# Optimization experiments

Measured on AMD Instinct MI355X. Metric: run time of the kernel, lower is better.

The kernel has to match this reference:

```python
import jax, jax.numpy as jnp
import numpy as np

N_NODES = 50000
N_EDGES = 600000
VOCAB = 50000
D_IN = 256   # embed.output_size
D = 128      # size


def gcn_conv(x, w, b, src, dst, num_nodes):
    # PyG GCNConv: x' = D^{-1/2} (A + I) D^{-1/2} (x @ W^T) + b
    loop = jnp.arange(num_nodes)
    s = jnp.concatenate([src, loop])
    d = jnp.concatenate([dst, loop])
    x = x @ w.T                                           # [N, D]
    deg = jax.ops.segment_sum(jnp.ones_like(s, x.dtype), d, num_segments=num_nodes)
    dinv = jnp.where(deg > 0, jax.lax.rsqrt(deg), 0.0)
    norm = dinv[s] * dinv[d]                              # [E+N]
    msgs = x[s] * norm[:, None]                           # gather + scale
    out = jax.ops.segment_sum(msgs, d, num_segments=num_nodes)  # scatter-add
    return out + b


def setup_inputs() -> dict:
    key = jax.random.key(0)
    ks = jax.random.split(key, 7)
    node_tokens = jax.random.randint(ks[0], (N_NODES,), 0, VOCAB)
    edge_index = jax.random.randint(ks[1], (2, N_EDGES), 0, N_NODES)
    embed_table = jax.random.normal(ks[2], (VOCAB, D_IN), dtype=jnp.float32) * 0.02
    W_node_w = jax.random.normal(ks[3], (D, D_IN), dtype=jnp.float32) * 0.02
    W_node_b = jnp.zeros((D,), dtype=jnp.float32)
    w1 = jax.random.normal(ks[4], (D, D), dtype=jnp.float32) * 0.02
    b1 = jnp.zeros((D,), dtype=jnp.float32)
    w2 = jax.random.normal(ks[5], (D, D), dtype=jnp.float32) * 0.02
    b2 = jnp.zeros((D,), dtype=jnp.float32)
    return {"node_tokens": node_tokens, "edge_index": edge_index,
            "embed_table": embed_table, "W_node_w": W_node_w, "W_node_b": W_node_b,
            "w1": w1, "b1": b1, "w2": w2, "b2": b2}


def reference(node_tokens, edge_index, embed_table, W_node_w, W_node_b, w1, b1, w2, b2):
    src, dst = edge_index[0], edge_index[1]
    e = embed_table[node_tokens]                 # [N, D_IN] embedding lookup
    x = e @ W_node_w.T + W_node_b                # [N, D]
    x = gcn_conv(x, w1, b1, src, dst, N_NODES)
    x = jax.nn.relu(x)
    x = gcn_conv(x, w2, b2, src, dst, N_NODES)
    return x
```

## Files before the change

kernel.cpp:

```cpp
#include <hip/hip_runtime.h>
#include <hip/hip_bf16.h>

#define N_NODES 50000
#define N_EDGES 600000
#define D_IN 256
#define D 128

#define SCAN_CHUNK 1024
#define N_CHUNKS ((N_NODES + SCAN_CHUNK - 1) / SCAN_CHUNK)
#define GEMM_BLOCKS ((N_NODES + 31) / 32)
#define EDGE_BLOCKS ((N_EDGES + 255) / 256)

typedef unsigned short ushort_t;
typedef __attribute__((ext_vector_type(8))) short bf16x8;
typedef __attribute__((ext_vector_type(16))) float f32x16;

__device__ __forceinline__ float bf2f(ushort_t u) {
  union { unsigned int i; float f; } v;
  v.i = ((unsigned int)u) << 16;
  return v.f;
}
__device__ __forceinline__ ushort_t f2bf(float f) {
  union { float f; unsigned int i; } v;
  v.f = f;
  unsigned int x = v.i;
  unsigned int r = (x + 0x7FFFu + ((x >> 16) & 1u)) >> 16;
  return (ushort_t)r;
}


__global__ __launch_bounds__(256) void k_prep_deg(
    const float* __restrict__ wn, const float* __restrict__ w1,
    const float* __restrict__ bn, const float* __restrict__ w2,
    const float* __restrict__ b1, const float* __restrict__ b2,
    const int* __restrict__ dst,
    ushort_t* __restrict__ WcSw, float* __restrict__ bc,
    ushort_t* __restrict__ W2Sw, float* __restrict__ b1f,
    float* __restrict__ b2f, int* __restrict__ deg,
    int* __restrict__ epos) {
  int bid = blockIdx.x;
  if (bid < 128) {
    int j = bid;
    int k = threadIdx.x;
    float acc = 0.f;
    for (int m = 0; m < 128; m++)
      acc += w1[j * 128 + m] * wn[m * 256 + k];
    ushort_t h = f2bf(acc);
    ushort_t l = f2bf(acc - bf2f(h));
    int wv = j >> 5, fm = j & 31;
    int kh = k >> 7, t = (k >> 4) & 7, fq = (k >> 3) & 1, c = k & 7;
    int lane = fq * 32 + fm;
    int base = ((wv * 2 + kh) * 8 + t) * 2 * 512 + lane * 8 + c;
    WcSw[base] = h;
    WcSw[base + 512] = l;
    if (k == 0) {
      float s = 0.f;
      for (int m = 0; m < 128; m++) s += w1[j * 128 + m] * bn[m];
      bc[j] = s;
    }
  } else if (bid < 193) {
    int i = (bid - 128) * 256 + threadIdx.x;
    if (i >= 16640) return;
    if (i < 16384) {
      float v = w2[i];
      ushort_t h = f2bf(v);
      ushort_t l = f2bf(v - bf2f(h));
      int j = i >> 7, k = i & 127;
      int wv = j >> 5, fm = j & 31;
      int t = (k >> 4) & 7, fq = (k >> 3) & 1, c = k & 7;
      int lane = fq * 32 + fm;
      int base = (wv * 8 + t) * 2 * 512 + lane * 8 + c;
      W2Sw[base] = h;
      W2Sw[base + 512] = l;
    } else if (i < 16512) {
      b1f[i - 16384] = b1[i - 16384];
    } else {
      b2f[i - 16512] = b2[i - 16512];
    }
  } else {
    int e = (bid - 193) * 256 + threadIdx.x;
    if (e < N_EDGES) epos[e] = atomicAdd(&deg[dst[e]], 1);
  }
}


__global__ void k_partial(const int* __restrict__ deg, int* __restrict__ partial) {
  __shared__ int lds[256];
  int b = blockIdx.x, t = threadIdx.x;
  int base = b * SCAN_CHUNK + t * 4;
  int s = 0;
#pragma unroll
  for (int i = 0; i < 4; i++) {
    int idx = base + i;
    if (idx < N_NODES) s += deg[idx];
  }
  lds[t] = s;
  __syncthreads();
  for (int off = 128; off > 0; off >>= 1) {
    if (t < off) lds[t] += lds[t + off];
    __syncthreads();
  }
  if (t == 0) partial[b] = lds[0];
}

__global__ void k_scan_final(const int* __restrict__ deg, const int* __restrict__ partial,
                             int* __restrict__ row_start, float* __restrict__ dinv) {
  __shared__ int lds[256];
  __shared__ int plds[64];
  int b = blockIdx.x, t = threadIdx.x;
  if (t < N_CHUNKS) plds[t] = partial[t];
  __syncthreads();
  if (t == 0) {
    int s = 0;
    for (int i = 0; i < b; i++) s += plds[i];
    plds[63] = s;
  }
  int base = b * SCAN_CHUNK + t * 4;
  int v[4];
  int s = 0;
#pragma unroll
  for (int i = 0; i < 4; i++) {
    int idx = base + i;
    v[i] = (idx < N_NODES) ? deg[idx] : 0;
    s += v[i];
  }
  lds[t] = s;
  __syncthreads();
  for (int off = 1; off < 256; off <<= 1) {
    int add = (t >= off) ? lds[t - off] : 0;
    __syncthreads();
    lds[t] += add;
    __syncthreads();
  }
  int excl = lds[t] - s + plds[63];
#pragma unroll
  for (int i = 0; i < 4; i++) {
    int idx = base + i;
    if (idx < N_NODES) {
      row_start[idx] = excl;
      dinv[idx] = rsqrtf((float)(v[i] + 1));
      excl += v[i];
    }
  }
  if (b == 0 && t == 0) row_start[N_NODES] = N_EDGES;
}

__global__ __launch_bounds__(256) void k_gemm_fill(
    const float* __restrict__ Xv, const int* __restrict__ tokens,
    const ushort_t* __restrict__ Wsw,
    const float* __restrict__ bias, const float* __restrict__ dinvp,
    ushort_t* __restrict__ OutT,
    const int* __restrict__ src, const int* __restrict__ dst,
    const int* __restrict__ row_start, const int* __restrict__ epos,
    int* __restrict__ csr) {
  constexpr int KDIM = D_IN;
  constexpr int KH = KDIM / 128;
  constexpr int XS = KDIM + 8;
  __shared__ __align__(16) ushort_t xh_lds[32 * XS];
  __shared__ __align__(16) ushort_t xl_lds[32 * XS];

  int bid = blockIdx.x;
  if (bid >= GEMM_BLOCKS) {
    int e = (bid - GEMM_BLOCKS) * 256 + threadIdx.x;
    if (e < N_EDGES) {
      int d = dst[e];
      csr[row_start[d] + epos[e]] = src[e];
    }
    return;
  }

  int tid = threadIdx.x;
  int lane = tid & 63;
  int wv = tid >> 6;
  int node0 = bid * 32;
  int fm = lane & 31;
  int fq = lane >> 5;

  {
    constexpr int NT = (32 * KDIM / 4) / 256;
    float4 v[NT];
    int rows[NT], cs[NT];
#pragma unroll
    for (int i = 0; i < NT; i++) {
      int seg = tid + 256 * i;
      rows[i] = seg / (KDIM / 4);
      cs[i] = seg % (KDIM / 4);
      int tk = tokens[min(node0 + rows[i], N_NODES - 1)];
      v[i] = *(const float4*)&Xv[(size_t)tk * KDIM + 4 * cs[i]];
    }
#pragma unroll
    for (int i = 0; i < NT; i++) {
      ushort4 h, l;
      h.x = f2bf(v[i].x); l.x = f2bf(v[i].x - bf2f(h.x));
      h.y = f2bf(v[i].y); l.y = f2bf(v[i].y - bf2f(h.y));
      h.z = f2bf(v[i].z); l.z = f2bf(v[i].z - bf2f(h.z));
      h.w = f2bf(v[i].w); l.w = f2bf(v[i].w - bf2f(h.w));
      *(ushort4*)&xh_lds[rows[i] * XS + 4 * cs[i]] = h;
      *(ushort4*)&xl_lds[rows[i] * XS + 4 * cs[i]] = l;
    }
  }
  __syncthreads();

  f32x16 acc;
#pragma unroll
  for (int r = 0; r < 16; r++) acc[r] = 0.f;

#pragma unroll
  for (int kh = 0; kh < KH; kh++) {
    const ushort_t* wb = Wsw + ((size_t)(wv * KH + kh) * 8) * 2 * 512 + lane * 8;
    bf16x8 wbh[8], wbl[8];
#pragma unroll
    for (int t = 0; t < 8; t++) {
      wbh[t] = *(const bf16x8*)(wb + (size_t)t * 1024);
      wbl[t] = *(const bf16x8*)(wb + (size_t)t * 1024 + 512);
    }
#pragma unroll
    for (int t = 0; t < 8; t++) {
      int ko = kh * 128 + t * 16 + fq * 8;
      bf16x8 ah = *(const bf16x8*)&xh_lds[fm * XS + ko];
      bf16x8 al = *(const bf16x8*)&xl_lds[fm * XS + ko];
      acc = __builtin_amdgcn_mfma_f32_32x32x16_bf16(ah, wbh[t], acc, 0, 0, 0);
      acc = __builtin_amdgcn_mfma_f32_32x32x16_bf16(ah, wbl[t], acc, 0, 0, 0);
      acc = __builtin_amdgcn_mfma_f32_32x32x16_bf16(al, wbh[t], acc, 0, 0, 0);
    }
  }
  int j = wv * 32 + fm;
  float bv = bias[j];
#pragma unroll
  for (int r = 0; r < 16; r++) {
    int row = (r & 3) + 8 * (r >> 2) + 4 * fq;
    int node = node0 + row;
    if (node < N_NODES)
      OutT[(size_t)node * D + j] = f2bf((acc[r] + bv) * dinvp[node]);
  }
}

__device__ __forceinline__ void addu4(float acc[8], uint4 u) {
  acc[0] += bf2f((ushort_t)(u.x & 0xFFFFu));
  acc[1] += bf2f((ushort_t)(u.x >> 16));
  acc[2] += bf2f((ushort_t)(u.y & 0xFFFFu));
  acc[3] += bf2f((ushort_t)(u.y >> 16));
  acc[4] += bf2f((ushort_t)(u.z & 0xFFFFu));
  acc[5] += bf2f((ushort_t)(u.z >> 16));
  acc[6] += bf2f((ushort_t)(u.w & 0xFFFFu));
  acc[7] += bf2f((ushort_t)(u.w >> 16));
}

__device__ __forceinline__ void agg_group(
    const uint4* __restrict__ tu4, const int* __restrict__ csr,
    int e0, int e1, int lane, int h, float acc[8]) {
  int gbase = lane & 48;
  for (int base = e0; base < e1; base += 16) {
    int cnt = min(16, e1 - base);
    int sidx = (h < cnt) ? csr[base + h] : 0;
    int i = 0;
    for (; i + 8 <= cnt; i += 8) {
      uint4 u[8];
#pragma unroll
      for (int q = 0; q < 8; q++) {
        int s = __shfl(sidx, gbase + i + q);
        u[q] = tu4[(size_t)s * 16 + h];
      }
#pragma unroll
      for (int q = 0; q < 8; q++) addu4(acc, u[q]);
    }
    if (i + 4 <= cnt) {
      uint4 u[4];
#pragma unroll
      for (int q = 0; q < 4; q++) {
        int s = __shfl(sidx, gbase + i + q);
        u[q] = tu4[(size_t)s * 16 + h];
      }
#pragma unroll
      for (int q = 0; q < 4; q++) addu4(acc, u[q]);
      i += 4;
    }
    if (i + 2 <= cnt) {
      uint4 u[2];
#pragma unroll
      for (int q = 0; q < 2; q++) {
        int s = __shfl(sidx, gbase + i + q);
        u[q] = tu4[(size_t)s * 16 + h];
      }
      addu4(acc, u[0]);
      addu4(acc, u[1]);
      i += 2;
    }
    if (i < cnt) {
      int s = __shfl(sidx, gbase + i);
      uint4 u = tu4[(size_t)s * 16 + h];
      addu4(acc, u);
    }
  }
}

__global__ __launch_bounds__(256) void k_agg_gemm(
    const ushort_t* __restrict__ t1, const int* __restrict__ row_start,
    const int* __restrict__ csr, const float* __restrict__ dinv,
    const float* __restrict__ b1f,
    const ushort_t* __restrict__ Wsw, ushort_t* __restrict__ OutT2) {
  constexpr int XS = 136;
  __shared__ __align__(16) ushort_t xh_lds[32 * XS];
  __shared__ __align__(16) ushort_t xl_lds[32 * XS];

  int tid = threadIdx.x;
  int lane = tid & 63;
  int wv = tid >> 6;
  int node0 = blockIdx.x * 32;
  int fm = lane & 31;
  int fq = lane >> 5;
  int g = lane >> 4;
  int h = lane & 15;

  const uint4* tu4 = (const uint4*)t1;
  float4 bA = *(const float4*)&b1f[h * 8];
  float4 bB = *(const float4*)&b1f[h * 8 + 4];

  int node0w = node0 + wv * 8;
  int rsv = row_start[min(node0w + min(lane, 8), N_NODES)];

#pragma unroll
  for (int p = 0; p < 2; p++) {
    int r = p * 4 + g;
    int row = wv * 8 + r;
    int node = node0 + row;
    int e0 = __shfl(rsv, r);
    int e1 = __shfl(rsv, r + 1);
    float acc[8];
#pragma unroll
    for (int q = 0; q < 8; q++) acc[q] = 0.f;
    if (node < N_NODES) {
      agg_group(tu4, csr, e0, e1, lane, h, acc);
      addu4(acc, tu4[(size_t)node * 16 + h]);
    }
    bf16x8 ph, pl;
    if (node < N_NODES) {
      float di = dinv[node];
      float v[8];
      v[0] = fmaxf(di * acc[0] + bA.x, 0.f);
      v[1] = fmaxf(di * acc[1] + bA.y, 0.f);
      v[2] = fmaxf(di * acc[2] + bA.z, 0.f);
      v[3] = fmaxf(di * acc[3] + bA.w, 0.f);
      v[4] = fmaxf(di * acc[4] + bB.x, 0.f);
      v[5] = fmaxf(di * acc[5] + bB.y, 0.f);
      v[6] = fmaxf(di * acc[6] + bB.z, 0.f);
      v[7] = fmaxf(di * acc[7] + bB.w, 0.f);
#pragma unroll
      for (int q = 0; q < 8; q++) {
        ushort_t hq = f2bf(v[q]);
        ph[q] = (short)hq;
        pl[q] = (short)f2bf(v[q] - bf2f(hq));
      }
    } else {
#pragma unroll
      for (int q = 0; q < 8; q++) { ph[q] = 0; pl[q] = 0; }
    }
    *(bf16x8*)&xh_lds[row * XS + h * 8] = ph;
    *(bf16x8*)&xl_lds[row * XS + h * 8] = pl;
  }
  __syncthreads();

  f32x16 acc;
#pragma unroll
  for (int r = 0; r < 16; r++) acc[r] = 0.f;
  {
    const ushort_t* wb = Wsw + ((size_t)wv * 8) * 2 * 512 + lane * 8;
    bf16x8 wbh[8], wbl[8];
#pragma unroll
    for (int t = 0; t < 8; t++) {
      wbh[t] = *(const bf16x8*)(wb + (size_t)t * 1024);
      wbl[t] = *(const bf16x8*)(wb + (size_t)t * 1024 + 512);
    }
#pragma unroll
    for (int t = 0; t < 8; t++) {
      int ko = t * 16 + fq * 8;
      bf16x8 ah = *(const bf16x8*)&xh_lds[fm * XS + ko];
      bf16x8 al = *(const bf16x8*)&xl_lds[fm * XS + ko];
      acc = __builtin_amdgcn_mfma_f32_32x32x16_bf16(ah, wbh[t], acc, 0, 0, 0);
      acc = __builtin_amdgcn_mfma_f32_32x32x16_bf16(ah, wbl[t], acc, 0, 0, 0);
      acc = __builtin_amdgcn_mfma_f32_32x32x16_bf16(al, wbh[t], acc, 0, 0, 0);
    }
  }
  int j = wv * 32 + fm;
#pragma unroll
  for (int r = 0; r < 16; r++) {
    int row = (r & 3) + 8 * (r >> 2) + 4 * fq;
    int node = node0 + row;
    if (node < N_NODES)
      OutT2[(size_t)node * D + j] = f2bf(acc[r] * dinv[node]);
  }
}

__global__ __launch_bounds__(256) void k_aggregate_out(
    const ushort_t* __restrict__ t, const int* __restrict__ row_start,
    const int* __restrict__ csr, const float* __restrict__ dinv,
    const float* __restrict__ bias, float* __restrict__ out_f) {
  int wv = threadIdx.x >> 6;
  int lane = threadIdx.x & 63;
  int g = lane >> 4;
  int h = lane & 15;
  int nodew = blockIdx.x * 16 + wv * 4;
  int rsv = row_start[min(nodew + min(lane, 4), N_NODES)];
  int node = nodew + g;
  int e0 = __shfl(rsv, g);
  int e1 = __shfl(rsv, g + 1);
  if (node >= N_NODES) return;

  const uint4* tu4 = (const uint4*)t;
  float acc[8];
#pragma unroll
  for (int q = 0; q < 8; q++) acc[q] = 0.f;
  agg_group(tu4, csr, e0, e1, lane, h, acc);
  addu4(acc, tu4[(size_t)node * 16 + h]);
  float di = dinv[node];
  float4 bA = *(const float4*)&bias[h * 8];
  float4 bB = *(const float4*)&bias[h * 8 + 4];
  float4 o0, o1;
  o0.x = di * acc[0] + bA.x;
  o0.y = di * acc[1] + bA.y;
  o0.z = di * acc[2] + bA.z;
  o0.w = di * acc[3] + bA.w;
  o1.x = di * acc[4] + bB.x;
  o1.y = di * acc[5] + bB.y;
  o1.z = di * acc[6] + bB.z;
  o1.w = di * acc[7] + bB.w;
  *(float4*)&out_f[(size_t)node * D + h * 8] = o0;
  *(float4*)&out_f[(size_t)node * D + h * 8 + 4] = o1;
}

extern "C" void kernel_launch(void* const* d_in, const int* in_sizes, int n_in,
                              void* d_out, int out_size, void* d_ws, size_t ws_size,
                              hipStream_t stream) {
  const int* tokens = (const int*)d_in[0];
  const int* edge = (const int*)d_in[1];
  const float* embed = (const float*)d_in[2];
  const float* Wn = (const float*)d_in[3];
  const float* bn = (const float*)d_in[4];
  const float* w1 = (const float*)d_in[5];
  const float* b1 = (const float*)d_in[6];
  const float* w2 = (const float*)d_in[7];
  const float* b2 = (const float*)d_in[8];
  float* out = (float*)d_out;

  const int* src = edge;
  const int* dst = edge + N_EDGES;

  char* ws = (char*)d_ws;
  ushort_t* T1 = (ushort_t*)ws;
  ushort_t* T2 = (ushort_t*)(ws + 12800000);
  int* epos = (int*)(ws + 25600000);
  float* dinv = (float*)(ws + 38400000);
  int* row_start = (int*)(ws + 38600064);
  int* deg = (int*)(ws + 38800128);
  int* csr = (int*)(ws + 39200128);
  int* partial = (int*)(ws + 41600192);
  ushort_t* WcSw = (ushort_t*)(ws + 41600512);
  ushort_t* W2Sw = (ushort_t*)(ws + 41731584);
  float* bias_ws = (float*)(ws + 41797120);
  float* bcf = bias_ws;
  float* b1f = bias_ws + 128;
  float* b2f = bias_ws + 256;

  hipMemsetAsync(deg, 0, N_NODES * sizeof(int), stream);
  k_prep_deg<<<193 + EDGE_BLOCKS, 256, 0, stream>>>(
      Wn, w1, bn, w2, b1, b2, dst, WcSw, bcf, W2Sw, b1f, b2f, deg, epos);

  k_partial<<<N_CHUNKS, 256, 0, stream>>>(deg, partial);
  k_scan_final<<<N_CHUNKS, 256, 0, stream>>>(deg, partial, row_start, dinv);

  k_gemm_fill<<<GEMM_BLOCKS + EDGE_BLOCKS, 256, 0, stream>>>(
      embed, tokens, WcSw, bcf, dinv, T1, src, dst, row_start, epos, csr);

  k_agg_gemm<<<GEMM_BLOCKS, 256, 0, stream>>>(
      T1, row_start, csr, dinv, b1f, W2Sw, T2);

  k_aggregate_out<<<(N_NODES + 15) / 16, 256, 0, stream>>>(
      T2, row_start, csr, dinv, b2f, out);
}
```

Measured before the change: 232.3 us.

## Add zero sentinel rows and unconditional 16-wide gather bursts in aggregation

Adds a zero padding row at index N_NODES in T1 and T2, written by the scan kernel, so aggregation can always issue a full 16-edge burst of gathers and pad missing edges with the sentinel index. The variable-length 8/4/2/1 gather tail is removed. Self-loop rows, dinv and CSR indices are prefetched up front, and the two nodes per group in k_agg_gemm are processed with independent accumulators. The embedding GEMM now splits its K dimension into two 128-wide LDS halves, which halves LDS use at the cost of an extra barrier. Bf16 unpacking uses cheaper mask/shift helpers. The risk is wasted bandwidth on padded loads for low-degree nodes and higher register pressure.

```diff
diff --git a/kernel.cpp b/kernel.cpp
--- a/kernel.cpp
+++ b/kernel.cpp
@@ -26,6 +26,16 @@
   unsigned int x = v.i;
   unsigned int r = (x + 0x7FFFu + ((x >> 16) & 1u)) >> 16;
   return (ushort_t)r;
+}
+__device__ __forceinline__ float bflo(unsigned int u) {
+  union { unsigned int i; float f; } v;
+  v.i = u << 16;
+  return v.f;
+}
+__device__ __forceinline__ float bfhi(unsigned int u) {
+  union { unsigned int i; float f; } v;
+  v.i = u & 0xFFFF0000u;
+  return v.f;
 }
 
 
@@ -104,7 +114,8 @@
 }
 
 __global__ void k_scan_final(const int* __restrict__ deg, const int* __restrict__ partial,
-                             int* __restrict__ row_start, float* __restrict__ dinv) {
+                             int* __restrict__ row_start, float* __restrict__ dinv,
+                             ushort_t* __restrict__ T1z, ushort_t* __restrict__ T2z) {
   __shared__ int lds[256];
   __shared__ int plds[64];
   int b = blockIdx.x, t = threadIdx.x;
@@ -142,7 +153,13 @@
       excl += v[i];
     }
   }
-  if (b == 0 && t == 0) row_start[N_NODES] = N_EDGES;
+  if (b == 0) {
+    if (t == 0) row_start[N_NODES] = N_EDGES;
+    unsigned int* z1 = (unsigned int*)&T1z[(size_t)N_NODES * D];
+    unsigned int* z2 = (unsigned int*)&T2z[(size_t)N_NODES * D];
+    if (t < 64) z1[t] = 0u;
+    else if (t < 128) z2[t - 64] = 0u;
+  }
 }
 
 __global__ __launch_bounds__(256) void k_gemm_fill(
@@ -153,9 +170,7 @@
     const int* __restrict__ src, const int* __restrict__ dst,
     const int* __restrict__ row_start, const int* __restrict__ epos,
     int* __restrict__ csr) {
-  constexpr int KDIM = D_IN;
-  constexpr int KH = KDIM / 128;
-  constexpr int XS = KDIM + 8;
+  constexpr int XS = 136;
   __shared__ __align__(16) ushort_t xh_lds[32 * XS];
   __shared__ __align__(16) ushort_t xl_lds[32 * XS];
 
@@ -175,39 +190,40 @@
   int node0 = bid * 32;
   int fm = lane & 31;
   int fq = lane >> 5;
-
-  {
-    constexpr int NT = (32 * KDIM / 4) / 256;
-    float4 v[NT];
-    int rows[NT], cs[NT];
-#pragma unroll
-    for (int i = 0; i < NT; i++) {
-      int seg = tid + 256 * i;
-      rows[i] = seg / (KDIM / 4);
-      cs[i] = seg % (KDIM / 4);
-      int tk = tokens[min(node0 + rows[i], N_NODES - 1)];
-      v[i] = *(const float4*)&Xv[(size_t)tk * KDIM + 4 * cs[i]];
-    }
-#pragma unroll
-    for (int i = 0; i < NT; i++) {
+  int r8 = tid >> 5;
+  int c32 = tid & 31;
+
+  float4 v0[4], v1[4];
+  int rows[4];
+#pragma unroll
+  for (int i = 0; i < 4; i++) {
+    rows[i] = r8 * 4 + i;
+    int tk = tokens[min(node0 + rows[i], N_NODES - 1)];
+    const float* rp = &Xv[(size_t)tk * D_IN];
+    v0[i] = *(const float4*)&rp[4 * c32];
+    v1[i] = *(const float4*)&rp[128 + 4 * c32];
+  }
+
+  f32x16 acc;
+#pragma unroll
+  for (int r = 0; r < 16; r++) acc[r] = 0.f;
+
+#pragma unroll
+  for (int kh = 0; kh < 2; kh++) {
+#pragma unroll
+    for (int i = 0; i < 4; i++) {
+      float4 v = (kh == 0) ? v0[i] : v1[i];
       ushort4 h, l;
-      h.x = f2bf(v[i].x); l.x = f2bf(v[i].x - bf2f(h.x));
-      h.y = f2bf(v[i].y); l.y = f2bf(v[i].y - bf2f(h.y));
-      h.z = f2bf(v[i].z); l.z = f2bf(v[i].z - bf2f(h.z));
-      h.w = f2bf(v[i].w); l.w = f2bf(v[i].w - bf2f(h.w));
-      *(ushort4*)&xh_lds[rows[i] * XS + 4 * cs[i]] = h;
-      *(ushort4*)&xl_lds[rows[i] * XS + 4 * cs[i]] = l;
-    }
-  }
-  __syncthreads();
-
-  f32x16 acc;
-#pragma unroll
-  for (int r = 0; r < 16; r++) acc[r] = 0.f;
-
-#pragma unroll
-  for (int kh = 0; kh < KH; kh++) {
-    const ushort_t* wb = Wsw + ((size_t)(wv * KH + kh) * 8) * 2 * 512 + lane * 8;
+      h.x = f2bf(v.x); l.x = f2bf(v.x - bf2f(h.x));
+      h.y = f2bf(v.y); l.y = f2bf(v.y - bf2f(h.y));
+      h.z = f2bf(v.z); l.z = f2bf(v.z - bf2f(h.z));
+      h.w = f2bf(v.w); l.w = f2bf(v.w - bf2f(h.w));
+      *(ushort4*)&xh_lds[rows[i] * XS + 4 * c32] = h;
+      *(ushort4*)&xl_lds[rows[i] * XS + 4 * c32] = l;
+    }
+    __syncthreads();
+
+    const ushort_t* wb = Wsw + ((size_t)(wv * 2 + kh) * 8) * 2 * 512 + lane * 8;
     bf16x8 wbh[8], wbl[8];
 #pragma unroll
     for (int t = 0; t < 8; t++) {
@@ -216,14 +232,16 @@
     }
 #pragma unroll
     for (int t = 0; t < 8; t++) {
-      int ko = kh * 128 + t * 16 + fq * 8;
+      int ko = t * 16 + fq * 8;
       bf16x8 ah = *(const bf16x8*)&xh_lds[fm * XS + ko];
       bf16x8 al = *(const bf16x8*)&xl_lds[fm * XS + ko];
       acc = __builtin_amdgcn_mfma_f32_32x32x16_bf16(ah, wbh[t], acc, 0, 0, 0);
       acc = __builtin_amdgcn_mfma_f32_32x32x16_bf16(ah, wbl[t], acc, 0, 0, 0);
       acc = __builtin_amdgcn_mfma_f32_32x32x16_bf16(al, wbh[t], acc, 0, 0, 0);
     }
-  }
+    if (kh == 0) __syncthreads();
+  }
+
   int j = wv * 32 + fm;
   float bv = bias[j];
 #pragma unroll
@@ -236,61 +254,36 @@
 }
 
 __device__ __forceinline__ void addu4(float acc[8], uint4 u) {
-  acc[0] += bf2f((ushort_t)(u.x & 0xFFFFu));
-  acc[1] += bf2f((ushort_t)(u.x >> 16));
-  acc[2] += bf2f((ushort_t)(u.y & 0xFFFFu));
-  acc[3] += bf2f((ushort_t)(u.y >> 16));
-  acc[4] += bf2f((ushort_t)(u.z & 0xFFFFu));
-  acc[5] += bf2f((ushort_t)(u.z >> 16));
-  acc[6] += bf2f((ushort_t)(u.w & 0xFFFFu));
-  acc[7] += bf2f((ushort_t)(u.w >> 16));
-}
-
-__device__ __forceinline__ void agg_group(
-    const uint4* __restrict__ tu4, const int* __restrict__ csr,
-    int e0, int e1, int lane, int h, float acc[8]) {
-  int gbase = lane & 48;
-  for (int base = e0; base < e1; base += 16) {
-    int cnt = min(16, e1 - base);
-    int sidx = (h < cnt) ? csr[base + h] : 0;
-    int i = 0;
-    for (; i + 8 <= cnt; i += 8) {
-      uint4 u[8];
-#pragma unroll
-      for (int q = 0; q < 8; q++) {
-        int s = __shfl(sidx, gbase + i + q);
-        u[q] = tu4[(size_t)s * 16 + h];
-      }
-#pragma unroll
-      for (int q = 0; q < 8; q++) addu4(acc, u[q]);
-    }
-    if (i + 4 <= cnt) {
-      uint4 u[4];
-#pragma unroll
-      for (int q = 0; q < 4; q++) {
-        int s = __shfl(sidx, gbase + i + q);
-        u[q] = tu4[(size_t)s * 16 + h];
-      }
-#pragma unroll
-      for (int q = 0; q < 4; q++) addu4(acc, u[q]);
-      i += 4;
-    }
-    if (i + 2 <= cnt) {
-      uint4 u[2];
-#pragma unroll
-      for (int q = 0; q < 2; q++) {
-        int s = __shfl(sidx, gbase + i + q);
-        u[q] = tu4[(size_t)s * 16 + h];
-      }
-      addu4(acc, u[0]);
-      addu4(acc, u[1]);
-      i += 2;
-    }
-    if (i < cnt) {
-      int s = __shfl(sidx, gbase + i);
-      uint4 u = tu4[(size_t)s * 16 + h];
-      addu4(acc, u);
-    }
+  acc[0] += bflo(u.x);
+  acc[1] += bfhi(u.x);
+  acc[2] += bflo(u.y);
+  acc[3] += bfhi(u.y);
+  acc[4] += bflo(u.z);
+  acc[5] += bfhi(u.z);
+  acc[6] += bflo(u.w);
+  acc[7] += bfhi(u.w);
+}
+
+__device__ __forceinline__ void burst16(const uint4* __restrict__ tu4, int sidx,
+                                        int gbase, int h, float acc[8]) {
+  uint4 u[16];
+#pragma unroll
+  for (int q = 0; q < 16; q++) {
+    int s = __shfl(sidx, gbase + q);
+    u[q] = tu4[(size_t)s * 16 + h];
+  }
+#pragma unroll
+  for (int q = 0; q < 16; q++) addu4(acc, u[q]);
+}
+
+__device__ __forceinline__ void agg_tail(const uint4* __restrict__ tu4,
+                                         const int* __restrict__ csr,
+                                         int e0, int e1, int gbase, int h,
+                                         float acc[8]) {
+  for (int b2 = e0 + 16; b2 < e1; b2 += 16) {
+    int c2 = e1 - b2;
+    int sx = (h < c2) ? csr[b2 + h] : N_NODES;
+    burst16(tu4, sx, gbase, h, acc);
   }
 }
 
@@ -311,6 +304,7 @@
   int fq = lane >> 5;
   int g = lane >> 4;
   int h = lane & 15;
+  int gbase = lane & 48;
 
   const uint4* tu4 = (const uint4*)t1;
   float4 bA = *(const float4*)&b1f[h * 8];
@@ -318,38 +312,58 @@
 
   int node0w = node0 + wv * 8;
   int rsv = row_start[min(node0w + min(lane, 8), N_NODES)];
+  float dvl = dinv[min(node0w + min(lane, 7), N_NODES - 1)];
+
+  int nodeA = node0w + g;
+  int nodeB = node0w + 4 + g;
+  int e0A = __shfl(rsv, g), e1A = __shfl(rsv, g + 1);
+  int e0B = __shfl(rsv, 4 + g), e1B = __shfl(rsv, 5 + g);
+  int cntA = e1A - e0A, cntB = e1B - e0B;
+  bool vA = nodeA < N_NODES, vB = nodeB < N_NODES;
+
+  int sidxA = (h < cntA) ? csr[e0A + h] : N_NODES;
+  int sidxB = (h < cntB) ? csr[e0B + h] : N_NODES;
+  uint4 usA = tu4[(size_t)(vA ? nodeA : N_NODES) * 16 + h];
+  uint4 usB = tu4[(size_t)(vB ? nodeB : N_NODES) * 16 + h];
+  float diA = __shfl(dvl, g);
+  float diB = __shfl(dvl, 4 + g);
+
+  float accA[8];
+#pragma unroll
+  for (int q = 0; q < 8; q++) accA[q] = 0.f;
+  addu4(accA, usA);
+  burst16(tu4, sidxA, gbase, h, accA);
+  agg_tail(tu4, csr, e0A, e1A, gbase, h, accA);
+
+  float accB[8];
+#pragma unroll
+  for (int q = 0; q < 8; q++) accB[q] = 0.f;
+  addu4(accB, usB);
+  burst16(tu4, sidxB, gbase, h, accB);
+  agg_tail(tu4, csr, e0B, e1B, gbase, h, accB);
 
 #pragma unroll
   for (int p = 0; p < 2; p++) {
-    int r = p * 4 + g;
-    int row = wv * 8 + r;
-    int node = node0 + row;
-    int e0 = __shfl(rsv, r);
-    int e1 = __shfl(rsv, r + 1);
-    float acc[8];
-#pragma unroll
-    for (int q = 0; q < 8; q++) acc[q] = 0.f;
-    if (node < N_NODES) {
-      agg_group(tu4, csr, e0, e1, lane, h, acc);
-      addu4(acc, tu4[(size_t)node * 16 + h]);
-    }
+    float* acc = p ? accB : accA;
+    bool vv = p ? vB : vA;
+    float di = p ? diB : diA;
+    int row = wv * 8 + p * 4 + g;
     bf16x8 ph, pl;
-    if (node < N_NODES) {
-      float di = dinv[node];
-      float v[8];
-      v[0] = fmaxf(di * acc[0] + bA.x, 0.f);
-      v[1] = fmaxf(di * acc[1] + bA.y, 0.f);
-      v[2] = fmaxf(di * acc[2] + bA.z, 0.f);
-      v[3] = fmaxf(di * acc[3] + bA.w, 0.f);
-      v[4] = fmaxf(di * acc[4] + bB.x, 0.f);
-      v[5] = fmaxf(di * acc[5] + bB.y, 0.f);
-      v[6] = fmaxf(di * acc[6] + bB.z, 0.f);
-      v[7] = fmaxf(di * acc[7] + bB.w, 0.f);
+    if (vv) {
+      float val[8];
+      val[0] = fmaxf(di * acc[0] + bA.x, 0.f);
+      val[1] = fmaxf(di * acc[1] + bA.y, 0.f);
+      val[2] = fmaxf(di * acc[2] + bA.z, 0.f);
+      val[3] = fmaxf(di * acc[3] + bA.w, 0.f);
+      val[4] = fmaxf(di * acc[4] + bB.x, 0.f);
+      val[5] = fmaxf(di * acc[5] + bB.y, 0.f);
+      val[6] = fmaxf(di * acc[6] + bB.z, 0.f);
+      val[7] = fmaxf(di * acc[7] + bB.w, 0.f);
 #pragma unroll
       for (int q = 0; q < 8; q++) {
-        ushort_t hq = f2bf(v[q]);
+        ushort_t hq = f2bf(val[q]);
         ph[q] = (short)hq;
-        pl[q] = (short)f2bf(v[q] - bf2f(hq));
+        pl[q] = (short)f2bf(val[q] - bf2f(hq));
       }
     } else {
 #pragma unroll
@@ -399,20 +413,28 @@
   int lane = threadIdx.x & 63;
   int g = lane >> 4;
   int h = lane & 15;
+  int gbase = lane & 48;
   int nodew = blockIdx.x * 16 + wv * 4;
   int rsv = row_start[min(nodew + min(lane, 4), N_NODES)];
+  float dvl = dinv[min(nodew + min(lane, 3), N_NODES - 1)];
   int node = nodew + g;
-  int e0 = __shfl(rsv, g);
-  int e1 = __shfl(rsv, g + 1);
-  if (node >= N_NODES) return;
+  int e0 = __shfl(rsv, g), e1 = __shfl(rsv, g + 1);
+  int cnt = e1 - e0;
+  bool vn = node < N_NODES;
 
   const uint4* tu4 = (const uint4*)t;
+  int sidx = (h < cnt) ? csr[e0 + h] : N_NODES;
+  uint4 us = tu4[(size_t)(vn ? node : N_NODES) * 16 + h];
+  float di = __shfl(dvl, g);
+
   float acc[8];
 #pragma unroll
   for (int q = 0; q < 8; q++) acc[q] = 0.f;
-  agg_group(tu4, csr, e0, e1, lane, h, acc);
-  addu4(acc, tu4[(size_t)node * 16 + h]);
-  float di = dinv[node];
+  addu4(acc, us);
+  burst16(tu4, sidx, gbase, h, acc);
+  agg_tail(tu4, csr, e0, e1, gbase, h, acc);
+
+  if (!vn) return;
   float4 bA = *(const float4*)&bias[h * 8];
   float4 bB = *(const float4*)&bias[h * 8 + 4];
   float4 o0, o1;
@@ -447,16 +469,16 @@
 
   char* ws = (char*)d_ws;
   ushort_t* T1 = (ushort_t*)ws;
-  ushort_t* T2 = (ushort_t*)(ws + 12800000);
-  int* epos = (int*)(ws + 25600000);
-  float* dinv = (float*)(ws + 38400000);
-  int* row_start = (int*)(ws + 38600064);
-  int* deg = (int*)(ws + 38800128);
-  int* csr = (int*)(ws + 39200128);
-  int* partial = (int*)(ws + 41600192);
-  ushort_t* WcSw = (ushort_t*)(ws + 41600512);
-  ushort_t* W2Sw = (ushort_t*)(ws + 41731584);
-  float* bias_ws = (float*)(ws + 41797120);
+  ushort_t* T2 = (ushort_t*)(ws + 12800256);
+  int* epos = (int*)(ws + 25600512);
+  float* dinv = (float*)(ws + 28000512);
+  int* row_start = (int*)(ws + 28200512);
+  int* deg = (int*)(ws + 28400576);
+  int* csr = (int*)(ws + 28600576);
+  int* partial = (int*)(ws + 31000576);
+  ushort_t* WcSw = (ushort_t*)(ws + 31000832);
+  ushort_t* W2Sw = (ushort_t*)(ws + 31131904);
+  float* bias_ws = (float*)(ws + 31197440);
   float* bcf = bias_ws;
   float* b1f = bias_ws + 128;
   float* b2f = bias_ws + 256;
@@ -466,7 +488,7 @@
       Wn, w1, bn, w2, b1, b2, dst, WcSw, bcf, W2Sw, b1f, b2f, deg, epos);
 
   k_partial<<<N_CHUNKS, 256, 0, stream>>>(deg, partial);
-  k_scan_final<<<N_CHUNKS, 256, 0, stream>>>(deg, partial, row_start, dinv);
+  k_scan_final<<<N_CHUNKS, 256, 0, stream>>>(deg, partial, row_start, dinv, T1, T2);
 
   k_gemm_fill<<<GEMM_BLOCKS + EDGE_BLOCKS, 256, 0, stream>>>(
       embed, tokens, WcSw, bcf, dinv, T1, src, dst, row_start, epos, csr);
```

Result: no change. 231.4 us (-0.4%).
